# Kernel optimization log

Hardware: AMD Instinct MI355X
Metric: run time of the kernel (lower is better)

Reference implementation:

```python
import jax, jax.numpy as jnp
import numpy as np

N, E, DIN, DOUT, NNZ = 8192, 4096, 256, 128, 65536
TEMP = float(DOUT) ** 0.5
NEG = -1e9


def setup_inputs() -> dict:
    key = jax.random.key(0)
    ks = jax.random.split(key, 8)
    stdv = 1.0 / np.sqrt(DOUT)
    u = lambda k, shp: jax.random.uniform(k, shp, jnp.float32, -stdv, stdv)
    x = jax.random.normal(ks[0], (N, DIN), jnp.float32)
    nodes = jax.random.randint(ks[1], (NNZ,), 0, N, jnp.int32)
    edges = jax.random.randint(ks[2], (NNZ,), 0, E, jnp.int32)
    hyperedge_index = jnp.stack([nodes, edges])  # [2, nnz]
    return {
        "x": x,
        "weight": u(ks[3], (DIN, DOUT)),   # transfer weight
        "weight2": u(ks[4], (DIN, DOUT)),
        "weight3": u(ks[5], (DOUT, DOUT)),
        "bias": u(ks[6], (DOUT,)),
        "q_ctx": u(ks[7], (DOUT,)),        # word_context.weight[0]
        "hyperedge_index": hyperedge_index,
        "num_nodes": N,
        "num_edges": E,
    }


def reference(x, weight, weight2, weight3, bias, q_ctx, hyperedge_index, num_nodes, num_edges):
    # dense incidence H[node, edge] = 1  (hyperedge_preprocess)
    H = jnp.zeros((num_nodes, num_edges), x.dtype).at[
        hyperedge_index[0], hyperedge_index[1]].set(1.0)
    adj = H.T                       # [E, N]  (mask / original attention for attn1)

    x4 = x @ weight2                # [N, D]  x_4att
    xt = x @ weight + bias          # [N, D]  transferred features (v of attn1)

    # ---- attention1: query = shared word-context vector, keys = x4 ----
    row = (q_ctx / TEMP) @ x4.T                    # [N] (q1 rows are identical)
    scores1 = jnp.where(adj == 0, NEG, row[None, :])  # [E, N]
    att1 = jax.nn.softmax(adj, axis=-1) + jax.nn.softmax(scores1, axis=-1)
    edge = att1 @ xt                               # [E, D]

    att2he = att1.T                                # [N, E]

    # ---- attention2: queries = x4, keys = edge @ W3 ----
    edge4 = edge @ weight3                         # [E, D]
    scores2 = jnp.where(adj.T == 0, NEG, (x4 / TEMP) @ edge4.T)  # [N, E]
    att2hn = jax.nn.softmax(adj.T, axis=-1) + jax.nn.softmax(scores2, axis=-1)

    # ---- fused outer-product attention and output projection ----
    A = att2he @ att2he.T + att2hn @ att2hn.T      # [N, N]
    h_prime_g = jax.nn.elu(A @ x4)                 # [N, D]
    return h_prime_g
```

## Files before the change

### kernel.cpp

```cpp
#include <hip/hip_runtime.h>
#include <math.h>

constexpr int Nn   = 8192;
constexpr int Ee   = 4096;
constexpr int DIN  = 256;
constexpr int DOUT = 128;
constexpr int NNZ  = 65536;
constexpr int EC   = 96;
constexpr int NC   = 48;

#define TEMPR 0.08838834764831845f
#define EM1   1.7182818284590452f

typedef __attribute__((ext_vector_type(8))) short short8;
typedef __attribute__((ext_vector_type(4))) float f32x4;

static __device__ __forceinline__ float wave_sum64(float v) {
#pragma unroll
    for (int m = 32; m; m >>= 1) v += __shfl_xor(v, m, 64);
    return v;
}
static __device__ __forceinline__ float wave_max64(float v) {
#pragma unroll
    for (int m = 32; m; m >>= 1) v = fmaxf(v, __shfl_xor(v, m, 64));
    return v;
}
static __device__ __forceinline__ short f2bf(float f) {
    union { float f; unsigned u; } v; v.f = f;
    const unsigned r = (v.u + 0x7FFFu + ((v.u >> 16) & 1u)) >> 16;
    return (short)r;
}
static __device__ __forceinline__ unsigned packbf2(float a, float b) {
    return ((unsigned)(unsigned short)f2bf(a)) |
           (((unsigned)(unsigned short)f2bf(b)) << 16);
}
static __device__ __forceinline__ float2 unpackbf2(unsigned u) {
    union { unsigned u; float f; } lo, hi;
    lo.u = u << 16; hi.u = u & 0xFFFF0000u;
    return make_float2(lo.f, hi.f);
}

__global__ __launch_bounds__(256) void k_ww3(
    const float* __restrict__ W, const float* __restrict__ W2,
    const float* __restrict__ W3, const float* __restrict__ bias,
    short* __restrict__ W2T, short* __restrict__ WWT, float* __restrict__ bW3,
    uint4* __restrict__ zb, unsigned zTot16)
{
    const int b = blockIdx.x;
    const int t = threadIdx.x;
    if (b < 32) {
        __shared__ float sW[8][128];
        const int r0 = b * 8;
        for (int i = t; i < 1024; i += 256)
            sW[i >> 7][i & 127] = W[(size_t)(r0 + (i >> 7)) * DOUT + (i & 127)];
        __syncthreads();
        const int c  = t & 127;
        const int rh = (t >> 7) * 4;
        float acc[4] = {0.f, 0.f, 0.f, 0.f};
        for (int k = 0; k < 128; ++k) {
            const float w3 = W3[(size_t)k * DOUT + c];
#pragma unroll
            for (int i = 0; i < 4; ++i) acc[i] = fmaf(sW[rh + i][k], w3, acc[i]);
        }
#pragma unroll
        for (int i = 0; i < 4; ++i)
            WWT[(size_t)c * DIN + (r0 + rh + i)] = f2bf(acc[i]);
    } else if (b < 40) {
        const int k0 = (b - 32) * 32;
        for (int i = t; i < 32 * 128; i += 256) {
            const int k = k0 + (i >> 7);
            const int n = i & 127;
            W2T[(size_t)n * DIN + k] = f2bf(W2[(size_t)k * DOUT + n]);
        }
    } else if (b == 40) {
        if (t < 128) {
            float acc = 0.f;
            for (int k = 0; k < 128; ++k)
                acc = fmaf(bias[k], W3[(size_t)k * DOUT + t], acc);
            bW3[t] = acc;
        }
    } else {
        uint4 z; z.x = z.y = z.z = z.w = 0u;
        for (unsigned i = (unsigned)(b - 41) * 256u + t; i < zTot16;
             i += 64u * 256u)
            zb[i] = z;
    }
}

__global__ __launch_bounds__(256) void k_gemm1f(
    const float* __restrict__ x, const short* __restrict__ W2T,
    const short* __restrict__ WWT, const float* __restrict__ bW3,
    const float* __restrict__ q, const int* __restrict__ hidx,
    unsigned* __restrict__ bitmap, int* __restrict__ degE, int* __restrict__ degN,
    int* __restrict__ csrEn, int* __restrict__ csrNe, int* __restrict__ csrNs,
    short* __restrict__ x4b, short* __restrict__ xwb,
    float* __restrict__ rowv, float* __restrict__ csx4, float* __restrict__ csxw)
{
    __shared__ float s4[DOUT], sw[DOUT], srow[16];
    const int t    = threadIdx.x;
    const int lane = t & 63;
    const int wv   = t >> 6;
    const int n16  = lane & 15;
    const int quad = lane >> 4;
    const int r0   = blockIdx.x * 16;
    const int n0   = wv * 32;

    const unsigned gid = blockIdx.x * 256 + t;
    if (gid < NNZ) {
        const int n = hidx[gid];
        const int e = hidx[NNZ + gid];
        const unsigned word = (unsigned)n * (unsigned)Ee + (unsigned)e;
        const unsigned bit  = 1u << (word & 31u);
        const unsigned old  = atomicOr(&bitmap[word >> 5], bit);
        if (!(old & bit)) {
            const int pe = atomicAdd(&degE[e], 1);
            if (pe < EC) {
                csrEn[e * EC + pe] = n;
                const int pn = atomicAdd(&degN[n], 1);
                if (pn < NC) {
                    csrNe[n * NC + pn] = e;
                    csrNs[n * NC + pn] = e * EC + pe;
                }
            }
        }
    }

    f32x4 acc4[2], accw[2];
#pragma unroll
    for (int nt = 0; nt < 2; ++nt) {
        acc4[nt] = (f32x4){0.f, 0.f, 0.f, 0.f};
        accw[nt] = (f32x4){0.f, 0.f, 0.f, 0.f};
    }
#pragma unroll
    for (int k0 = 0; k0 < DIN; k0 += 32) {
        const int kb = k0 + quad * 8;
        const float4 xa = *(const float4*)&x[(size_t)(r0 + n16) * DIN + kb];
        const float4 xb = *(const float4*)&x[(size_t)(r0 + n16) * DIN + kb + 4];
        short8 af;
        af[0] = f2bf(xa.x); af[1] = f2bf(xa.y); af[2] = f2bf(xa.z); af[3] = f2bf(xa.w);
        af[4] = f2bf(xb.x); af[5] = f2bf(xb.y); af[6] = f2bf(xb.z); af[7] = f2bf(xb.w);
#pragma unroll
        for (int nt = 0; nt < 2; ++nt) {
            const int col = n0 + nt * 16 + n16;
            const short8 b4 = *(const short8*)&W2T[(size_t)col * DIN + kb];
            const short8 bw = *(const short8*)&WWT[(size_t)col * DIN + kb];
            acc4[nt] = __builtin_amdgcn_mfma_f32_16x16x32_bf16(af, b4, acc4[nt], 0, 0, 0);
            accw[nt] = __builtin_amdgcn_mfma_f32_16x16x32_bf16(af, bw, accw[nt], 0, 0, 0);
        }
    }

    float bwv[2], qv[2];
#pragma unroll
    for (int nt = 0; nt < 2; ++nt) {
        const int col = n0 + nt * 16 + n16;
        bwv[nt] = bW3[col];
        qv[nt]  = q[col];
    }
#pragma unroll
    for (int nt = 0; nt < 2; ++nt) {
        const int col = n0 + nt * 16 + n16;
#pragma unroll
        for (int reg = 0; reg < 4; ++reg) {
            const int row = r0 + quad * 4 + reg;
            x4b[(size_t)row * DOUT + col] = f2bf(acc4[nt][reg]);
            xwb[(size_t)row * DOUT + col] = f2bf(accw[nt][reg] + bwv[nt]);
        }
    }
    float pr[4];
#pragma unroll
    for (int reg = 0; reg < 4; ++reg)
        pr[reg] = qv[0] * acc4[0][reg] + qv[1] * acc4[1][reg];
#pragma unroll
    for (int m = 8; m; m >>= 1) {
#pragma unroll
        for (int reg = 0; reg < 4; ++reg) pr[reg] += __shfl_xor(pr[reg], m, 64);
    }
    if (t < 16) srow[t] = 0.f;
    if (t < DOUT) { s4[t] = 0.f; sw[t] = 0.f; }
    __syncthreads();
    if (n16 == 0) {
#pragma unroll
        for (int reg = 0; reg < 4; ++reg) atomicAdd(&srow[quad * 4 + reg], pr[reg]);
    }
#pragma unroll
    for (int nt = 0; nt < 2; ++nt) {
        const int col = n0 + nt * 16 + n16;
        const float c4s = acc4[nt][0] + acc4[nt][1] + acc4[nt][2] + acc4[nt][3];
        const float cws = accw[nt][0] + accw[nt][1] + accw[nt][2] + accw[nt][3]
                        + 4.f * bwv[nt];
        atomicAdd(&s4[col], c4s);
        atomicAdd(&sw[col], cws);
    }
    __syncthreads();
    if (t < 16) rowv[r0 + t] = srow[t] * TEMPR;
    if (t < DOUT) { atomicAdd(&csx4[t], s4[t]); atomicAdd(&csxw[t], sw[t]); }
}

__global__ __launch_bounds__(256) void k_edge1(
    const int* __restrict__ degE, const int* __restrict__ csrEn,
    const float* __restrict__ rowv,
    const float* __restrict__ csx4, const float* __restrict__ csxw,
    const unsigned* __restrict__ x4b, const unsigned* __restrict__ xwb,
    float* __restrict__ Sval, unsigned* __restrict__ e4b, unsigned* __restrict__ G1b,
    float* __restrict__ wsArr, float* __restrict__ c2g)
{
    __shared__ int   sN[4][EC];
    __shared__ float sS[4][EC];
    __shared__ float sC2[4];
    const int t    = threadIdx.x;
    const int w    = t >> 6;
    const int lane = t & 63;
    const int e    = blockIdx.x * 4 + w;
    const int deg  = min(degE[e], EC);
    const float ue = deg ? 1.0f / ((float)Nn + (float)deg * EM1) : 2.0f / (float)Nn;

    int   n0 = 0, n1 = 0;
    float r0 = -INFINITY, r1 = -INFINITY;
    if (lane < deg)      { n0 = csrEn[e * EC + lane];      r0 = rowv[n0]; }
    if (lane + 64 < deg) { n1 = csrEn[e * EC + lane + 64]; r1 = rowv[n1]; }
    const float m  = wave_max64(fmaxf(r0, r1));
    const float e0 = (lane < deg)      ? expf(r0 - m) : 0.f;
    const float e1 = (lane + 64 < deg) ? expf(r1 - m) : 0.f;
    const float Z  = wave_sum64(e0 + e1);
    const float inv = deg ? 1.0f / Z : 0.f;
    const float base = EM1 * ue;
    if (lane < deg) {
        const float sv = fmaf(e0, inv, base);
        sN[w][lane] = n0; sS[w][lane] = sv;
        Sval[e * EC + lane] = sv;
        atomicAdd(&wsArr[n0], ue * sv);
    }
    if (lane + 64 < deg) {
        const float sv = fmaf(e1, inv, base);
        sN[w][lane + 64] = n1; sS[w][lane + 64] = sv;
        Sval[e * EC + lane + 64] = sv;
        atomicAdd(&wsArr[n1], ue * sv);
    }

    const float2 cw = *(const float2*)&csxw[lane * 2];
    const float2 c4 = *(const float2*)&csx4[lane * 2];
    float2 aE = make_float2(ue * cw.x, ue * cw.y);
    float2 aG = make_float2(ue * c4.x, ue * c4.y);
    int j = 0;
    for (; j + 8 <= deg; j += 8) {
        int ai[8]; float bi[8]; unsigned tu[8], fu[8];
#pragma unroll
        for (int k = 0; k < 8; ++k) { ai[k] = sN[w][j+k]; bi[k] = sS[w][j+k]; }
#pragma unroll
        for (int k = 0; k < 8; ++k) {
            tu[k] = xwb[(size_t)ai[k] * 64 + lane];
            fu[k] = x4b[(size_t)ai[k] * 64 + lane];
        }
#pragma unroll
        for (int k = 0; k < 8; ++k) {
            const float2 tv = unpackbf2(tu[k]);
            const float2 fv = unpackbf2(fu[k]);
            aE.x = fmaf(bi[k], tv.x, aE.x); aE.y = fmaf(bi[k], tv.y, aE.y);
            aG.x = fmaf(bi[k], fv.x, aG.x); aG.y = fmaf(bi[k], fv.y, aG.y);
        }
    }
    for (; j < deg; ++j) {
        const int   a = sN[w][j];
        const float b = sS[w][j];
        const float2 tv = unpackbf2(xwb[(size_t)a * 64 + lane]);
        const float2 fv = unpackbf2(x4b[(size_t)a * 64 + lane]);
        aE.x = fmaf(b, tv.x, aE.x); aE.y = fmaf(b, tv.y, aE.y);
        aG.x = fmaf(b, fv.x, aG.x); aG.y = fmaf(b, fv.y, aG.y);
    }
    e4b[(size_t)e * 64 + lane] = packbf2(aE.x, aE.y);
    G1b[(size_t)e * 64 + lane] = packbf2(aG.x, aG.y);

    if (lane == 0) sC2[w] = ue * ue;
    __syncthreads();
    if (t == 0) atomicAdd(c2g, sC2[0] + sC2[1] + sC2[2] + sC2[3]);
}

__global__ __launch_bounds__(256) void k_node2(
    const int* __restrict__ degN, const int* __restrict__ csrNe,
    const int* __restrict__ csrNs, const unsigned* __restrict__ x4b,
    const unsigned* __restrict__ e4b, const float* __restrict__ wsArr,
    float* __restrict__ Tval, float* __restrict__ vArr,
    float* __restrict__ vxg, float* __restrict__ twxg, float* __restrict__ wsxg)
{
    __shared__ float sx[4][DOUT];
    __shared__ float sVX[DOUT], sTX[DOUT], sWX[DOUT];
    const int t    = threadIdx.x;
    const int w    = t >> 6;
    const int lane = t & 63;

    float2 vxa = {0,0}, twa = {0,0}, wsa = {0,0};
#pragma unroll
    for (int s = 0; s < 2; ++s) {
        const int n   = blockIdx.x * 8 + w * 2 + s;
        const int deg = min(degN[n], NC);
        const float vn = deg ? 1.0f / ((float)Ee + (float)deg * EM1) : 2.0f / (float)Ee;
        const float2 xv = unpackbf2(x4b[(size_t)n * 64 + lane]);
        sx[w][lane * 2 + 0] = xv.x;
        sx[w][lane * 2 + 1] = xv.y;
        __builtin_amdgcn_s_waitcnt(0);
        int ej = 0, slot = 0;
        if (lane < deg) { ej = csrNe[n * NC + lane]; slot = csrNs[n * NC + lane]; }
        const uint4* er = (const uint4*)&e4b[(size_t)ej * 64];
        float dot = 0.f;
#pragma unroll
        for (int c0 = 0; c0 < 16; c0 += 8) {
            uint4 ev[8];
#pragma unroll
            for (int k = 0; k < 8; ++k) ev[k] = er[c0 + k];
#pragma unroll
            for (int k = 0; k < 8; ++k) {
                const int base = (c0 + k) * 8;
                const float2 e0 = unpackbf2(ev[k].x);
                const float2 e1 = unpackbf2(ev[k].y);
                const float2 e2 = unpackbf2(ev[k].z);
                const float2 e3 = unpackbf2(ev[k].w);
                dot = fmaf(e0.x, sx[w][base + 0], dot);
                dot = fmaf(e0.y, sx[w][base + 1], dot);
                dot = fmaf(e1.x, sx[w][base + 2], dot);
                dot = fmaf(e1.y, sx[w][base + 3], dot);
                dot = fmaf(e2.x, sx[w][base + 4], dot);
                dot = fmaf(e2.y, sx[w][base + 5], dot);
                dot = fmaf(e3.x, sx[w][base + 6], dot);
                dot = fmaf(e3.y, sx[w][base + 7], dot);
            }
        }
        const float sj = (lane < deg) ? dot * TEMPR : -INFINITY;
        const float m  = wave_max64(sj);
        const float ex = (lane < deg) ? expf(sj - m) : 0.f;
        const float Z  = wave_sum64(ex);
        if (lane < deg) Tval[slot] = fmaf(EM1, vn, ex / Z);
        if (lane == 0) vArr[n] = vn;
        const float tw  = deg ? fmaf((float)deg * EM1, vn, 1.0f) : 0.f;
        const float wsn = wsArr[n];
        vxa.x = fmaf(vn,  xv.x, vxa.x); vxa.y = fmaf(vn,  xv.y, vxa.y);
        twa.x = fmaf(tw,  xv.x, twa.x); twa.y = fmaf(tw,  xv.y, twa.y);
        wsa.x = fmaf(wsn, xv.x, wsa.x); wsa.y = fmaf(wsn, xv.y, wsa.y);
    }
    __syncthreads();
    if (t < DOUT) { sVX[t] = 0.f; sTX[t] = 0.f; sWX[t] = 0.f; }
    __syncthreads();
    atomicAdd(&sVX[lane*2+0], vxa.x); atomicAdd(&sVX[lane*2+1], vxa.y);
    atomicAdd(&sTX[lane*2+0], twa.x); atomicAdd(&sTX[lane*2+1], twa.y);
    atomicAdd(&sWX[lane*2+0], wsa.x); atomicAdd(&sWX[lane*2+1], wsa.y);
    __syncthreads();
    if (t < DOUT) {
        atomicAdd(&vxg[t],  sVX[t]);
        atomicAdd(&twxg[t], sTX[t]);
        atomicAdd(&wsxg[t], sWX[t]);
    }
}

__global__ __launch_bounds__(256) void k_g2(
    const int* __restrict__ degE, const int* __restrict__ csrEn,
    const float* __restrict__ Tval, const float* __restrict__ vxg,
    const unsigned* __restrict__ x4b, unsigned* __restrict__ G2b)
{
    const int t    = threadIdx.x;
    const int w    = t >> 6;
    const int lane = t & 63;
    const int e    = blockIdx.x * 4 + w;
    const int deg  = min(degE[e], EC);
    float2 acc = *(const float2*)&vxg[lane * 2];
    int j = 0;
    for (; j + 8 <= deg; j += 8) {
        int ai[8]; float bi[8]; unsigned fu[8];
#pragma unroll
        for (int k = 0; k < 8; ++k) { ai[k] = csrEn[e*EC+j+k]; bi[k] = Tval[e*EC+j+k]; }
#pragma unroll
        for (int k = 0; k < 8; ++k)
            fu[k] = x4b[(size_t)ai[k] * 64 + lane];
#pragma unroll
        for (int k = 0; k < 8; ++k) {
            const float2 fv = unpackbf2(fu[k]);
            acc.x = fmaf(bi[k], fv.x, acc.x); acc.y = fmaf(bi[k], fv.y, acc.y);
        }
    }
    for (; j < deg; ++j) {
        const int   a = csrEn[e*EC+j];
        const float b = Tval[e*EC+j];
        const float2 fv = unpackbf2(x4b[(size_t)a * 64 + lane]);
        acc.x = fmaf(b, fv.x, acc.x); acc.y = fmaf(b, fv.y, acc.y);
    }
    G2b[(size_t)e * 64 + lane] = packbf2(acc.x, acc.y);
}

__global__ __launch_bounds__(256) void k_final(
    const int* __restrict__ degN, const int* __restrict__ csrNe,
    const int* __restrict__ csrNs, const float* __restrict__ Sval,
    const float* __restrict__ Tval, const float* __restrict__ vArr,
    const float* __restrict__ c2g, const float* __restrict__ csx4,
    const float* __restrict__ wsxg, const float* __restrict__ vxg,
    const float* __restrict__ twxg,
    const unsigned* __restrict__ G1b, const unsigned* __restrict__ G2b,
    float* __restrict__ out)
{
    const int t    = threadIdx.x;
    const int w    = t >> 6;
    const int lane = t & 63;
    const int n    = blockIdx.x * 4 + w;
    const int deg  = min(degN[n], NC);
    const float vn = vArr[n];
    const float c2 = *c2g;
    const float2 c4v = *(const float2*)&csx4[lane * 2];
    const float2 wsv = *(const float2*)&wsxg[lane * 2];
    const float2 vxv = *(const float2*)&vxg[lane * 2];
    const float2 twv = *(const float2*)&twxg[lane * 2];
    float2 acc;
    acc.x = fmaf(c2, c4v.x, wsv.x) + vn * fmaf((float)Ee, vxv.x, twv.x);
    acc.y = fmaf(c2, c4v.y, wsv.y) + vn * fmaf((float)Ee, vxv.y, twv.y);
    int j = 0;
    for (; j + 4 <= deg; j += 4) {
        int ei[4], si[4]; float sv[4], tv[4]; unsigned g1u[4], g2u[4];
#pragma unroll
        for (int k = 0; k < 4; ++k) {
            ei[k] = csrNe[n*NC+j+k]; si[k] = csrNs[n*NC+j+k];
        }
#pragma unroll
        for (int k = 0; k < 4; ++k) {
            sv[k] = Sval[si[k]]; tv[k] = Tval[si[k]];
            g1u[k] = G1b[(size_t)ei[k] * 64 + lane];
            g2u[k] = G2b[(size_t)ei[k] * 64 + lane];
        }
#pragma unroll
        for (int k = 0; k < 4; ++k) {
            const float2 g1 = unpackbf2(g1u[k]);
            const float2 g2 = unpackbf2(g2u[k]);
            acc.x = fmaf(sv[k], g1.x, acc.x); acc.y = fmaf(sv[k], g1.y, acc.y);
            acc.x = fmaf(tv[k], g2.x, acc.x); acc.y = fmaf(tv[k], g2.y, acc.y);
        }
    }
    for (; j < deg; ++j) {
        const int ea = csrNe[n*NC+j];
        const int sa = csrNs[n*NC+j];
        const float sva = Sval[sa], tva = Tval[sa];
        const float2 g1a = unpackbf2(G1b[(size_t)ea * 64 + lane]);
        const float2 g2a = unpackbf2(G2b[(size_t)ea * 64 + lane]);
        acc.x = fmaf(sva, g1a.x, acc.x); acc.y = fmaf(sva, g1a.y, acc.y);
        acc.x = fmaf(tva, g2a.x, acc.x); acc.y = fmaf(tva, g2a.y, acc.y);
    }
    acc.x = acc.x > 0.f ? acc.x : expm1f(acc.x);
    acc.y = acc.y > 0.f ? acc.y : expm1f(acc.y);
    *(float2*)&out[(size_t)n * DOUT + lane * 2] = acc;
}

extern "C" void kernel_launch(void* const* d_in, const int* in_sizes, int n_in,
                              void* d_out, int out_size, void* d_ws, size_t ws_size,
                              hipStream_t stream)
{
    const float* x    = (const float*)d_in[0];
    const float* W    = (const float*)d_in[1];
    const float* W2   = (const float*)d_in[2];
    const float* W3   = (const float*)d_in[3];
    const float* bias = (const float*)d_in[4];
    const float* q    = (const float*)d_in[5];
    const int*   hidx = (const int*)d_in[6];
    float* out = (float*)d_out;

    char* wsp = (char*)d_ws;
    size_t o = 0;
    auto take = [&](size_t bytes) {
        size_t r = o; o += (bytes + 255) & ~(size_t)255; return r;
    };
    unsigned* bitmap = (unsigned*)(wsp + take((size_t)Nn * Ee / 8));
    int*   degE  = (int*)  (wsp + take((size_t)Ee * 4));
    int*   degN  = (int*)  (wsp + take((size_t)Nn * 4));
    float* wsArr = (float*)(wsp + take((size_t)Nn * 4));
    float* c2g   = (float*)(wsp + take(4));
    float* csx4  = (float*)(wsp + take(DOUT * 4));
    float* csxw  = (float*)(wsp + take(DOUT * 4));
    float* vxg   = (float*)(wsp + take(DOUT * 4));
    float* twxg  = (float*)(wsp + take(DOUT * 4));
    float* wsxg  = (float*)(wsp + take(DOUT * 4));
    const size_t zbytes = o;
    short* x4b   = (short*)(wsp + take((size_t)Nn * DOUT * 2));
    short* xwb   = (short*)(wsp + take((size_t)Nn * DOUT * 2));
    float* rowv  = (float*)(wsp + take((size_t)Nn * 4));
    float* vArr  = (float*)(wsp + take((size_t)Nn * 4));
    int*   csrEn = (int*)  (wsp + take((size_t)Ee * EC * 4));
    float* Sval  = (float*)(wsp + take((size_t)Ee * EC * 4));
    float* Tval  = (float*)(wsp + take((size_t)Ee * EC * 4));
    int*   csrNe = (int*)  (wsp + take((size_t)Nn * NC * 4));
    int*   csrNs = (int*)  (wsp + take((size_t)Nn * NC * 4));
    unsigned* e4b = (unsigned*)(wsp + take((size_t)Ee * DOUT * 2));
    unsigned* G1b = (unsigned*)(wsp + take((size_t)Ee * DOUT * 2));
    unsigned* G2b = (unsigned*)(wsp + take((size_t)Ee * DOUT * 2));
    short* W2T   = (short*)(wsp + take((size_t)DOUT * DIN * 2));
    short* WWT   = (short*)(wsp + take((size_t)DOUT * DIN * 2));
    float* bW3   = (float*)(wsp + take(DOUT * 4));
    (void)ws_size; (void)in_sizes; (void)n_in; (void)out_size;

    k_ww3   <<<105,     256, 0, stream>>>(W, W2, W3, bias, W2T, WWT, bW3,
                                          (uint4*)d_ws, (unsigned)(zbytes / 16));
    k_gemm1f<<<Nn / 16, 256, 0, stream>>>(x, W2T, WWT, bW3, q, hidx,
                                          bitmap, degE, degN, csrEn, csrNe, csrNs,
                                          x4b, xwb, rowv, csx4, csxw);
    k_edge1 <<<Ee / 4,  256, 0, stream>>>(degE, csrEn, rowv, csx4, csxw,
                                          (const unsigned*)x4b, (const unsigned*)xwb,
                                          Sval, e4b, G1b, wsArr, c2g);
    k_node2 <<<Nn / 8,  256, 0, stream>>>(degN, csrNe, csrNs,
                                          (const unsigned*)x4b, e4b, wsArr,
                                          Tval, vArr, vxg, twxg, wsxg);
    k_g2    <<<Ee / 4,  256, 0, stream>>>(degE, csrEn, Tval, vxg,
                                          (const unsigned*)x4b, G2b);
    k_final <<<Nn / 4,  256, 0, stream>>>(degN, csrNe, csrNs, Sval, Tval, vArr,
                                          c2g, csx4, wsxg, vxg, twxg, G1b, G2b, out);
}
```

Baseline: 183.4 us.

## Split per-edge dot products across 8 lanes in node attention kernel

Restructures k_node2 so each wave handles one node, and each incident edge's 128-wide dot product is split across 8 lanes with coalesced uint4 loads and shuffle reductions. Previously one lane per edge read a full 256-byte row serially and took x from LDS. The softmax is now computed over up to six groups of 8 edges, and the grid doubles to Nn/4 blocks. The goals are better memory coalescing, more parallelism, and no LDS staging of x, at the cost of more shuffles and twice as many global atomics on the reduction buffers.

```diff
diff --git a/kernel.cpp b/kernel.cpp
--- a/kernel.cpp
+++ b/kernel.cpp
@@ -282,66 +282,83 @@
     float* __restrict__ Tval, float* __restrict__ vArr,
     float* __restrict__ vxg, float* __restrict__ twxg, float* __restrict__ wsxg)
 {
-    __shared__ float sx[4][DOUT];
     __shared__ float sVX[DOUT], sTX[DOUT], sWX[DOUT];
     const int t    = threadIdx.x;
     const int w    = t >> 6;
     const int lane = t & 63;
-
-    float2 vxa = {0,0}, twa = {0,0}, wsa = {0,0};
-#pragma unroll
-    for (int s = 0; s < 2; ++s) {
-        const int n   = blockIdx.x * 8 + w * 2 + s;
-        const int deg = min(degN[n], NC);
-        const float vn = deg ? 1.0f / ((float)Ee + (float)deg * EM1) : 2.0f / (float)Ee;
-        const float2 xv = unpackbf2(x4b[(size_t)n * 64 + lane]);
-        sx[w][lane * 2 + 0] = xv.x;
-        sx[w][lane * 2 + 1] = xv.y;
-        __builtin_amdgcn_s_waitcnt(0);
-        int ej = 0, slot = 0;
-        if (lane < deg) { ej = csrNe[n * NC + lane]; slot = csrNs[n * NC + lane]; }
+    const int es   = lane >> 3;
+    const int dl   = lane & 7;
+    const int n    = blockIdx.x * 4 + w;
+    const int deg  = min(degN[n], NC);
+    const float vn = deg ? 1.0f / ((float)Ee + (float)deg * EM1) : 2.0f / (float)Ee;
+
+    const uint4* xr = (const uint4*)&x4b[(size_t)n * 64];
+    const uint4 xua = xr[dl * 2], xub = xr[dl * 2 + 1];
+    const float2 x0 = unpackbf2(xua.x), x1 = unpackbf2(xua.y),
+                 x2 = unpackbf2(xua.z), x3 = unpackbf2(xua.w),
+                 x4v = unpackbf2(xub.x), x5 = unpackbf2(xub.y),
+                 x6 = unpackbf2(xub.z), x7 = unpackbf2(xub.w);
+
+    float dps[6]; float exs[6]; int slots[6];
+    float m = -INFINITY;
+#pragma unroll
+    for (int p = 0; p < 6; ++p) {
+        dps[p] = -INFINITY; slots[p] = 0;
+        if (p * 8 >= deg) continue;
+        const int j = p * 8 + es;
+        int ej = 0;
+        if (j < deg) { ej = csrNe[n * NC + j]; slots[p] = csrNs[n * NC + j]; }
         const uint4* er = (const uint4*)&e4b[(size_t)ej * 64];
-        float dot = 0.f;
-#pragma unroll
-        for (int c0 = 0; c0 < 16; c0 += 8) {
-            uint4 ev[8];
-#pragma unroll
-            for (int k = 0; k < 8; ++k) ev[k] = er[c0 + k];
-#pragma unroll
-            for (int k = 0; k < 8; ++k) {
-                const int base = (c0 + k) * 8;
-                const float2 e0 = unpackbf2(ev[k].x);
-                const float2 e1 = unpackbf2(ev[k].y);
-                const float2 e2 = unpackbf2(ev[k].z);
-                const float2 e3 = unpackbf2(ev[k].w);
-                dot = fmaf(e0.x, sx[w][base + 0], dot);
-                dot = fmaf(e0.y, sx[w][base + 1], dot);
-                dot = fmaf(e1.x, sx[w][base + 2], dot);
-                dot = fmaf(e1.y, sx[w][base + 3], dot);
-                dot = fmaf(e2.x, sx[w][base + 4], dot);
-                dot = fmaf(e2.y, sx[w][base + 5], dot);
-                dot = fmaf(e3.x, sx[w][base + 6], dot);
-                dot = fmaf(e3.y, sx[w][base + 7], dot);
-            }
-        }
-        const float sj = (lane < deg) ? dot * TEMPR : -INFINITY;
-        const float m  = wave_max64(sj);
-        const float ex = (lane < deg) ? expf(sj - m) : 0.f;
-        const float Z  = wave_sum64(ex);
-        if (lane < deg) Tval[slot] = fmaf(EM1, vn, ex / Z);
-        if (lane == 0) vArr[n] = vn;
-        const float tw  = deg ? fmaf((float)deg * EM1, vn, 1.0f) : 0.f;
-        const float wsn = wsArr[n];
-        vxa.x = fmaf(vn,  xv.x, vxa.x); vxa.y = fmaf(vn,  xv.y, vxa.y);
-        twa.x = fmaf(tw,  xv.x, twa.x); twa.y = fmaf(tw,  xv.y, twa.y);
-        wsa.x = fmaf(wsn, xv.x, wsa.x); wsa.y = fmaf(wsn, xv.y, wsa.y);
-    }
-    __syncthreads();
+        const uint4 ea = er[dl * 2], eb = er[dl * 2 + 1];
+        float d0 = 0.f, d1 = 0.f, d2 = 0.f, d3 = 0.f;
+        { const float2 ev = unpackbf2(ea.x); d0 = fmaf(ev.x, x0.x, d0); d0 = fmaf(ev.y, x0.y, d0); }
+        { const float2 ev = unpackbf2(ea.y); d1 = fmaf(ev.x, x1.x, d1); d1 = fmaf(ev.y, x1.y, d1); }
+        { const float2 ev = unpackbf2(ea.z); d2 = fmaf(ev.x, x2.x, d2); d2 = fmaf(ev.y, x2.y, d2); }
+        { const float2 ev = unpackbf2(ea.w); d3 = fmaf(ev.x, x3.x, d3); d3 = fmaf(ev.y, x3.y, d3); }
+        { const float2 ev = unpackbf2(eb.x); d0 = fmaf(ev.x, x4v.x, d0); d0 = fmaf(ev.y, x4v.y, d0); }
+        { const float2 ev = unpackbf2(eb.y); d1 = fmaf(ev.x, x5.x, d1); d1 = fmaf(ev.y, x5.y, d1); }
+        { const float2 ev = unpackbf2(eb.z); d2 = fmaf(ev.x, x6.x, d2); d2 = fmaf(ev.y, x6.y, d2); }
+        { const float2 ev = unpackbf2(eb.w); d3 = fmaf(ev.x, x7.x, d3); d3 = fmaf(ev.y, x7.y, d3); }
+        float dot = (d0 + d1) + (d2 + d3);
+        dot += __shfl_xor(dot, 1, 64);
+        dot += __shfl_xor(dot, 2, 64);
+        dot += __shfl_xor(dot, 4, 64);
+        dot = (j < deg) ? dot * TEMPR : -INFINITY;
+        dps[p] = dot;
+        float mm = fmaxf(dot, __shfl_xor(dot, 8, 64));
+        mm = fmaxf(mm, __shfl_xor(mm, 16, 64));
+        mm = fmaxf(mm, __shfl_xor(mm, 32, 64));
+        m = fmaxf(m, mm);
+    }
+    float Z = 0.f;
+#pragma unroll
+    for (int p = 0; p < 6; ++p) {
+        exs[p] = 0.f;
+        if (p * 8 >= deg) continue;
+        const float ex = (p * 8 + es < deg) ? expf(dps[p] - m) : 0.f;
+        exs[p] = ex;
+        float s = ex + __shfl_xor(ex, 8, 64);
+        s += __shfl_xor(s, 16, 64);
+        s += __shfl_xor(s, 32, 64);
+        Z += s;
+    }
+    const float invZ = deg ? 1.0f / Z : 0.f;
+#pragma unroll
+    for (int p = 0; p < 6; ++p) {
+        if (p * 8 >= deg) continue;
+        if (dl == 0 && p * 8 + es < deg)
+            Tval[slots[p]] = fmaf(EM1, vn, exs[p] * invZ);
+    }
+    if (lane == 0) vArr[n] = vn;
+
+    const float tw  = deg ? fmaf((float)deg * EM1, vn, 1.0f) : 0.f;
+    const float wsn = wsArr[n];
+    const float2 xv = unpackbf2(x4b[(size_t)n * 64 + lane]);
     if (t < DOUT) { sVX[t] = 0.f; sTX[t] = 0.f; sWX[t] = 0.f; }
     __syncthreads();
-    atomicAdd(&sVX[lane*2+0], vxa.x); atomicAdd(&sVX[lane*2+1], vxa.y);
-    atomicAdd(&sTX[lane*2+0], twa.x); atomicAdd(&sTX[lane*2+1], twa.y);
-    atomicAdd(&sWX[lane*2+0], wsa.x); atomicAdd(&sWX[lane*2+1], wsa.y);
+    atomicAdd(&sVX[lane*2+0], vn  * xv.x); atomicAdd(&sVX[lane*2+1], vn  * xv.y);
+    atomicAdd(&sTX[lane*2+0], tw  * xv.x); atomicAdd(&sTX[lane*2+1], tw  * xv.y);
+    atomicAdd(&sWX[lane*2+0], wsn * xv.x); atomicAdd(&sWX[lane*2+1], wsn * xv.y);
     __syncthreads();
     if (t < DOUT) {
         atomicAdd(&vxg[t],  sVX[t]);
@@ -497,7 +514,7 @@
     k_edge1 <<<Ee / 4,  256, 0, stream>>>(degE, csrEn, rowv, csx4, csxw,
                                           (const unsigned*)x4b, (const unsigned*)xwb,
                                           Sval, e4b, G1b, wsArr, c2g);
-    k_node2 <<<Nn / 8,  256, 0, stream>>>(degN, csrNe, csrNs,
+    k_node2 <<<Nn / 4,  256, 0, stream>>>(degN, csrNe, csrNs,
                                           (const unsigned*)x4b, e4b, wsArr,
                                           Tval, vArr, vxg, twxg, wsxg);
     k_g2    <<<Ee / 4,  256, 0, stream>>>(degE, csrEn, Tval, vxg,
```

Result: slower. 204.1 us (+11.3%).
